# Performance work log

Measured on AMD Instinct MI355X. Metric: run time of the kernel, lower is better.

## Reference

```python
import jax, jax.numpy as jnp
import numpy as np

N_NODES = 100000
N_EDGES = 3200000
D_IN = 128
D_H0 = 64
D_H1 = 32
N_GRAPHS = 1024
N_CLASSES = 16


def setup_inputs() -> dict:
    key = jax.random.key(0)
    ks = jax.random.split(key, 9)
    x = jax.random.normal(ks[0], (N_NODES, D_IN), dtype=jnp.float32)
    edge_index = jax.random.randint(ks[1], (2, N_EDGES), 0, N_NODES, dtype=jnp.int64)
    node_graph_index = jnp.sort(
        jax.random.randint(ks[2], (N_NODES,), 0, N_GRAPHS, dtype=jnp.int64))

    def glorot(k, shape):
        lim = np.sqrt(6.0 / (shape[0] + shape[1]))
        return jax.random.uniform(k, shape, jnp.float32, -lim, lim)

    W0 = glorot(ks[3], (D_IN, D_H0))
    b0 = jnp.zeros((D_H0,), jnp.float32)
    W1 = glorot(ks[4], (D_H0, D_H1))
    b1 = jnp.zeros((D_H1,), jnp.float32)
    Wd = glorot(ks[5], (D_H1, N_CLASSES))
    bd = jnp.zeros((N_CLASSES,), jnp.float32)
    return {"x": x, "edge_index": edge_index, "node_graph_index": node_graph_index,
            "W0": W0, "b0": b0, "W1": W1, "b1": b1, "Wd": Wd, "bd": bd}


def reference(x, edge_index, node_graph_index, W0, b0, W1, b1, Wd, bd):
    N = x.shape[0]
    # GCN renormalization: add self-loops, symmetric D^-1/2 (A+I) D^-1/2
    loops = jnp.arange(N, dtype=edge_index.dtype)
    row = jnp.concatenate([edge_index[0], loops])  # target nodes
    col = jnp.concatenate([edge_index[1], loops])  # source nodes
    deg = jax.ops.segment_sum(jnp.ones_like(row, dtype=x.dtype), row, num_segments=N)
    inv_sqrt = jax.lax.rsqrt(deg)  # deg >= 1 thanks to self-loops
    norm = inv_sqrt[row] * inv_sqrt[col]  # [E+N]

    def gcn(h, W, b):
        hW = h @ W                                   # [N, d_out]
        msg = hW[col] * norm[:, None]                # [E+N, d_out]
        agg = jax.ops.segment_sum(msg, row, num_segments=N)
        return jax.nn.relu(agg + b)

    h = gcn(x, W0, b0)          # [N, 64]  (dropout is identity at inference)
    h = gcn(h, W1, b1)          # [N, 32]

    # mean pool over graphs
    sums = jax.ops.segment_sum(h, node_graph_index, num_segments=N_GRAPHS)
    cnt = jax.ops.segment_sum(jnp.ones((N,), x.dtype), node_graph_index,
                              num_segments=N_GRAPHS)
    pooled = sums / jnp.maximum(cnt, 1.0)[:, None]   # [G, 32]
    return pooled @ Wd + bd                          # [G, n_classes]
```

## Files before the change

### kernel.cpp

```cpp
#include <hip/hip_runtime.h>

#define GSHIFT 9
#define GSIZE 512
#define MAXG 256
#define GCAP 17664
#define CHUNKA 4096

typedef unsigned short bfraw;

__device__ __forceinline__ bfraw f2bf(float f) {
    unsigned u = __float_as_uint(f);
    unsigned r = u + 0x7FFFu + ((u >> 16) & 1u);
    return (bfraw)(r >> 16);
}
__device__ __forceinline__ float bflo(unsigned u) { return __uint_as_float(u << 16); }
__device__ __forceinline__ float bfhi(unsigned u) { return __uint_as_float(u & 0xFFFF0000u); }


__global__ __launch_bounds__(256) void k_ginit(int* __restrict__ gcur, int ngroups) {
    int g = threadIdx.x;
    if (g < ngroups) gcur[g] = g * GCAP;
}

__global__ __launch_bounds__(512) void k_partA(const int* __restrict__ row,
                                               const int* __restrict__ col,
                                               int* __restrict__ gcur,
                                               int* __restrict__ gbuf, int E) {
    __shared__ int h[MAXG];
    __shared__ int base[MAXG];
    int tid = threadIdx.x;
    if (tid < MAXG) h[tid] = 0;
    __syncthreads();
    int start = blockIdx.x * CHUNKA;
    int end = min(E, start + CHUNKA);
    for (int i = start + tid; i < end; i += 512)
        atomicAdd(&h[row[i] >> GSHIFT], 1);
    __syncthreads();
    if (tid < MAXG) {
        int c = h[tid];
        base[tid] = c ? atomicAdd(&gcur[tid], c) : 0;
        h[tid] = 0;
    }
    __syncthreads();
    for (int i = start + tid; i < end; i += 512) {
        int r = row[i], c = col[i];
        int g = r >> GSHIFT;
        int p = base[g] + atomicAdd(&h[g], 1);
        if (p < (g + 1) * GCAP)
            gbuf[p] = ((r & (GSIZE - 1)) << 17) | c;
    }
}

__global__ __launch_bounds__(512) void k_partB(const int* __restrict__ gbuf,
                                               const int* __restrict__ gcur,
                                               int* __restrict__ off,
                                               int* __restrict__ off2,
                                               int* __restrict__ scol,
                                               float* __restrict__ invs, int N) {
    __shared__ int hist[GSIZE];
    __shared__ int lex[GSIZE];
    int g = blockIdx.x, tid = threadIdx.x;
    int nstart = g << GSHIFT;
    int s = g * GCAP;
    int cnt = min(gcur[g] - s, GCAP);
    hist[tid] = 0;
    __syncthreads();
    for (int k = tid; k < cnt; k += 512)
        atomicAdd(&hist[gbuf[s + k] >> 17], 1);
    __syncthreads();
    int d0 = hist[tid];
    lex[tid] = d0;
    __syncthreads();
    for (int d = 1; d < GSIZE; d <<= 1) {
        int a = (tid >= d) ? lex[tid - d] : 0;
        __syncthreads();
        lex[tid] += a;
        __syncthreads();
    }
    int st = s + lex[tid] - d0;
    int node = nstart + tid;
    if (node < N) {
        off[node] = st;
        off2[node] = st + d0;
        invs[node] = rsqrtf((float)(d0 + 1));
    }
    hist[tid] = st;
    __syncthreads();
    for (int k = tid; k < cnt; k += 512) {
        int p = gbuf[s + k];
        int pos = atomicAdd(&hist[p >> 17], 1);
        scol[pos] = p & 0x1FFFF;
    }
}


__global__ __launch_bounds__(256) void k_gemm0(const float* __restrict__ x,
                                               const float* __restrict__ W,
                                               const float* __restrict__ invs,
                                               bfraw* __restrict__ out, int N) {
    __shared__ float sW[128 * 64];
    for (int i = threadIdx.x; i < 2048; i += 256)
        ((float4*)sW)[i] = ((const float4*)W)[i];
    __syncthreads();
    int t = threadIdx.x;
    int tc = t & 15, tr = t >> 4;
    int rbase = blockIdx.x * 64 + tr * 4;
    float acc[4][4] = {};
    int rr[4];
#pragma unroll
    for (int i = 0; i < 4; ++i) rr[i] = min(rbase + i, N - 1);
    for (int k = 0; k < 128; k += 4) {
        float4 wv0 = *(const float4*)&sW[(k + 0) * 64 + tc * 4];
        float4 wv1 = *(const float4*)&sW[(k + 1) * 64 + tc * 4];
        float4 wv2 = *(const float4*)&sW[(k + 2) * 64 + tc * 4];
        float4 wv3 = *(const float4*)&sW[(k + 3) * 64 + tc * 4];
#pragma unroll
        for (int i = 0; i < 4; ++i) {
            float4 xv = *(const float4*)(x + (size_t)rr[i] * 128 + k);
            acc[i][0] = fmaf(xv.x, wv0.x, acc[i][0]);
            acc[i][1] = fmaf(xv.x, wv0.y, acc[i][1]);
            acc[i][2] = fmaf(xv.x, wv0.z, acc[i][2]);
            acc[i][3] = fmaf(xv.x, wv0.w, acc[i][3]);
            acc[i][0] = fmaf(xv.y, wv1.x, acc[i][0]);
            acc[i][1] = fmaf(xv.y, wv1.y, acc[i][1]);
            acc[i][2] = fmaf(xv.y, wv1.z, acc[i][2]);
            acc[i][3] = fmaf(xv.y, wv1.w, acc[i][3]);
            acc[i][0] = fmaf(xv.z, wv2.x, acc[i][0]);
            acc[i][1] = fmaf(xv.z, wv2.y, acc[i][1]);
            acc[i][2] = fmaf(xv.z, wv2.z, acc[i][2]);
            acc[i][3] = fmaf(xv.z, wv2.w, acc[i][3]);
            acc[i][0] = fmaf(xv.w, wv3.x, acc[i][0]);
            acc[i][1] = fmaf(xv.w, wv3.y, acc[i][1]);
            acc[i][2] = fmaf(xv.w, wv3.z, acc[i][2]);
            acc[i][3] = fmaf(xv.w, wv3.w, acc[i][3]);
        }
    }
#pragma unroll
    for (int i = 0; i < 4; ++i) {
        int row = rbase + i;
        if (row < N) {
            float iv = invs[row];
            ushort4 o;
            o.x = f2bf(iv * acc[i][0]);
            o.y = f2bf(iv * acc[i][1]);
            o.z = f2bf(iv * acc[i][2]);
            o.w = f2bf(iv * acc[i][3]);
            *(ushort4*)(out + (size_t)row * 64 + tc * 4) = o;
        }
    }
}

__global__ __launch_bounds__(256) void k_gemm1(const float* __restrict__ h,
                                               const float* __restrict__ W,
                                               const float* __restrict__ invs,
                                               bfraw* __restrict__ out, int N) {
    __shared__ float sW[64 * 32];
    for (int i = threadIdx.x; i < 512; i += 256)
        ((float4*)sW)[i] = ((const float4*)W)[i];
    __syncthreads();
    int t = threadIdx.x;
    int tc = t & 7, tr = t >> 3;
    int rbase = blockIdx.x * 128 + tr * 4;
    float acc[4][4] = {};
    int rr[4];
#pragma unroll
    for (int i = 0; i < 4; ++i) rr[i] = min(rbase + i, N - 1);
    for (int k = 0; k < 64; k += 4) {
        float4 wv0 = *(const float4*)&sW[(k + 0) * 32 + tc * 4];
        float4 wv1 = *(const float4*)&sW[(k + 1) * 32 + tc * 4];
        float4 wv2 = *(const float4*)&sW[(k + 2) * 32 + tc * 4];
        float4 wv3 = *(const float4*)&sW[(k + 3) * 32 + tc * 4];
#pragma unroll
        for (int i = 0; i < 4; ++i) {
            float4 xv = *(const float4*)(h + (size_t)rr[i] * 64 + k);
            acc[i][0] = fmaf(xv.x, wv0.x, acc[i][0]);
            acc[i][1] = fmaf(xv.x, wv0.y, acc[i][1]);
            acc[i][2] = fmaf(xv.x, wv0.z, acc[i][2]);
            acc[i][3] = fmaf(xv.x, wv0.w, acc[i][3]);
            acc[i][0] = fmaf(xv.y, wv1.x, acc[i][0]);
            acc[i][1] = fmaf(xv.y, wv1.y, acc[i][1]);
            acc[i][2] = fmaf(xv.y, wv1.z, acc[i][2]);
            acc[i][3] = fmaf(xv.y, wv1.w, acc[i][3]);
            acc[i][0] = fmaf(xv.z, wv2.x, acc[i][0]);
            acc[i][1] = fmaf(xv.z, wv2.y, acc[i][1]);
            acc[i][2] = fmaf(xv.z, wv2.z, acc[i][2]);
            acc[i][3] = fmaf(xv.z, wv2.w, acc[i][3]);
            acc[i][0] = fmaf(xv.w, wv3.x, acc[i][0]);
            acc[i][1] = fmaf(xv.w, wv3.y, acc[i][1]);
            acc[i][2] = fmaf(xv.w, wv3.z, acc[i][2]);
            acc[i][3] = fmaf(xv.w, wv3.w, acc[i][3]);
        }
    }
#pragma unroll
    for (int i = 0; i < 4; ++i) {
        int row = rbase + i;
        if (row < N) {
            float iv = invs[row];
            ushort4 o;
            o.x = f2bf(iv * acc[i][0]);
            o.y = f2bf(iv * acc[i][1]);
            o.z = f2bf(iv * acc[i][2]);
            o.w = f2bf(iv * acc[i][3]);
            *(ushort4*)(out + (size_t)row * 32 + tc * 4) = o;
        }
    }
}


__global__ __launch_bounds__(256) void k_agg64_w(const int* __restrict__ scol,
                                                 const int* __restrict__ off,
                                                 const int* __restrict__ off2,
                                                 const float* __restrict__ invs,
                                                 const bfraw* __restrict__ hWb,
                                                 const float* __restrict__ bias,
                                                 float* __restrict__ h0, int N) {
    int node = blockIdx.x * 4 + (threadIdx.x >> 6);
    if (node >= N) return;
    int lane = threadIdx.x & 63;
    int fl = lane & 7, sg = lane >> 3;
    int s = off[node], e = off2[node];
    float a[8] = {}, c[8] = {};
    int k = s + sg;
    for (; k + 24 < e; k += 32) {
        int n0 = scol[k], n1 = scol[k + 8], n2 = scol[k + 16], n3 = scol[k + 24];
        uint4 u0 = *(const uint4*)(hWb + (size_t)n0 * 64 + fl * 8);
        uint4 u1 = *(const uint4*)(hWb + (size_t)n1 * 64 + fl * 8);
        uint4 u2 = *(const uint4*)(hWb + (size_t)n2 * 64 + fl * 8);
        uint4 u3 = *(const uint4*)(hWb + (size_t)n3 * 64 + fl * 8);
        a[0] += bflo(u0.x); a[1] += bfhi(u0.x); a[2] += bflo(u0.y); a[3] += bfhi(u0.y);
        a[4] += bflo(u0.z); a[5] += bfhi(u0.z); a[6] += bflo(u0.w); a[7] += bfhi(u0.w);
        c[0] += bflo(u1.x); c[1] += bfhi(u1.x); c[2] += bflo(u1.y); c[3] += bfhi(u1.y);
        c[4] += bflo(u1.z); c[5] += bfhi(u1.z); c[6] += bflo(u1.w); c[7] += bfhi(u1.w);
        a[0] += bflo(u2.x); a[1] += bfhi(u2.x); a[2] += bflo(u2.y); a[3] += bfhi(u2.y);
        a[4] += bflo(u2.z); a[5] += bfhi(u2.z); a[6] += bflo(u2.w); a[7] += bfhi(u2.w);
        c[0] += bflo(u3.x); c[1] += bfhi(u3.x); c[2] += bflo(u3.y); c[3] += bfhi(u3.y);
        c[4] += bflo(u3.z); c[5] += bfhi(u3.z); c[6] += bflo(u3.w); c[7] += bfhi(u3.w);
    }
    for (; k < e; k += 8) {
        uint4 u = *(const uint4*)(hWb + (size_t)scol[k] * 64 + fl * 8);
        a[0] += bflo(u.x); a[1] += bfhi(u.x); a[2] += bflo(u.y); a[3] += bfhi(u.y);
        a[4] += bflo(u.z); a[5] += bfhi(u.z); a[6] += bflo(u.w); a[7] += bfhi(u.w);
    }
#pragma unroll
    for (int j = 0; j < 8; ++j) a[j] += c[j];
#pragma unroll
    for (int m = 8; m < 64; m <<= 1) {
#pragma unroll
        for (int j = 0; j < 8; ++j) a[j] += __shfl_xor(a[j], m, 64);
    }
    if (sg == 0) {
        uint4 u = *(const uint4*)(hWb + (size_t)node * 64 + fl * 8);
        float iv = invs[node];
        int fb = fl * 8;
        float4 o1, o2;
        o1.x = fmaxf(iv * (a[0] + bflo(u.x)) + bias[fb + 0], 0.f);
        o1.y = fmaxf(iv * (a[1] + bfhi(u.x)) + bias[fb + 1], 0.f);
        o1.z = fmaxf(iv * (a[2] + bflo(u.y)) + bias[fb + 2], 0.f);
        o1.w = fmaxf(iv * (a[3] + bfhi(u.y)) + bias[fb + 3], 0.f);
        o2.x = fmaxf(iv * (a[4] + bflo(u.z)) + bias[fb + 4], 0.f);
        o2.y = fmaxf(iv * (a[5] + bfhi(u.z)) + bias[fb + 5], 0.f);
        o2.z = fmaxf(iv * (a[6] + bflo(u.w)) + bias[fb + 6], 0.f);
        o2.w = fmaxf(iv * (a[7] + bfhi(u.w)) + bias[fb + 7], 0.f);
        *(float4*)(h0 + (size_t)node * 64 + fb) = o1;
        *(float4*)(h0 + (size_t)node * 64 + fb + 4) = o2;
    }
}

__global__ __launch_bounds__(256) void k_agg32_w(const int* __restrict__ scol,
                                                 const int* __restrict__ off,
                                                 const int* __restrict__ off2,
                                                 const float* __restrict__ invs,
                                                 const bfraw* __restrict__ hWb,
                                                 const float* __restrict__ bias,
                                                 float* __restrict__ h1, int N) {
    int node = blockIdx.x * 4 + (threadIdx.x >> 6);
    if (node >= N) return;
    int lane = threadIdx.x & 63;
    int fl = lane & 3, sg = lane >> 2;
    int s = off[node], e = off2[node];
    float a[8] = {}, c[8] = {};
    int k = s + sg;
    for (; k + 16 < e; k += 32) {
        int n0 = scol[k], n1 = scol[k + 16];
        uint4 u0 = *(const uint4*)(hWb + (size_t)n0 * 32 + fl * 8);
        uint4 u1 = *(const uint4*)(hWb + (size_t)n1 * 32 + fl * 8);
        a[0] += bflo(u0.x); a[1] += bfhi(u0.x); a[2] += bflo(u0.y); a[3] += bfhi(u0.y);
        a[4] += bflo(u0.z); a[5] += bfhi(u0.z); a[6] += bflo(u0.w); a[7] += bfhi(u0.w);
        c[0] += bflo(u1.x); c[1] += bfhi(u1.x); c[2] += bflo(u1.y); c[3] += bfhi(u1.y);
        c[4] += bflo(u1.z); c[5] += bfhi(u1.z); c[6] += bflo(u1.w); c[7] += bfhi(u1.w);
    }
    for (; k < e; k += 16) {
        uint4 u = *(const uint4*)(hWb + (size_t)scol[k] * 32 + fl * 8);
        a[0] += bflo(u.x); a[1] += bfhi(u.x); a[2] += bflo(u.y); a[3] += bfhi(u.y);
        a[4] += bflo(u.z); a[5] += bfhi(u.z); a[6] += bflo(u.w); a[7] += bfhi(u.w);
    }
#pragma unroll
    for (int j = 0; j < 8; ++j) a[j] += c[j];
#pragma unroll
    for (int m = 4; m < 64; m <<= 1) {
#pragma unroll
        for (int j = 0; j < 8; ++j) a[j] += __shfl_xor(a[j], m, 64);
    }
    if (sg == 0) {
        uint4 u = *(const uint4*)(hWb + (size_t)node * 32 + fl * 8);
        float iv = invs[node];
        int fb = fl * 8;
        float4 o1, o2;
        o1.x = fmaxf(iv * (a[0] + bflo(u.x)) + bias[fb + 0], 0.f);
        o1.y = fmaxf(iv * (a[1] + bfhi(u.x)) + bias[fb + 1], 0.f);
        o1.z = fmaxf(iv * (a[2] + bflo(u.y)) + bias[fb + 2], 0.f);
        o1.w = fmaxf(iv * (a[3] + bfhi(u.y)) + bias[fb + 3], 0.f);
        o2.x = fmaxf(iv * (a[4] + bflo(u.z)) + bias[fb + 4], 0.f);
        o2.y = fmaxf(iv * (a[5] + bfhi(u.z)) + bias[fb + 5], 0.f);
        o2.z = fmaxf(iv * (a[6] + bflo(u.w)) + bias[fb + 6], 0.f);
        o2.w = fmaxf(iv * (a[7] + bfhi(u.w)) + bias[fb + 7], 0.f);
        *(float4*)(h1 + (size_t)node * 32 + fb) = o1;
        *(float4*)(h1 + (size_t)node * 32 + fb + 4) = o2;
    }
}


__global__ __launch_bounds__(256) void k_gbound(const int* __restrict__ gidx,
                                                int* __restrict__ gstart,
                                                int N, int G) {
    int i = blockIdx.x * 256 + threadIdx.x;
    if (i > N) return;
    if (i == 0) {
        int g0 = gidx[0];
        for (int g = 0; g <= g0; ++g) gstart[g] = 0;
    } else if (i == N) {
        int gl = gidx[N - 1];
        for (int g = gl + 1; g <= G; ++g) gstart[g] = N;
    } else {
        int a = gidx[i - 1], b = gidx[i];
        for (int g = a + 1; g <= b; ++g) gstart[g] = i;
    }
}

__global__ __launch_bounds__(256) void k_pool_head(const float* __restrict__ h1,
                                                   const int* __restrict__ gstart,
                                                   const float* __restrict__ Wd,
                                                   const float* __restrict__ bd,
                                                   float* __restrict__ out) {
    int g = blockIdx.x;
    int s = gstart[g], e = gstart[g + 1];
    int tid = threadIdx.x;
    int lane = tid & 63, w = tid >> 6;
    int f = lane & 31, half = lane >> 5;
    float acc = 0.f;
    for (int n = s + w * 2 + half; n < e; n += 8)
        acc += h1[(size_t)n * 32 + f];
    acc += __shfl_xor(acc, 32, 64);
    __shared__ float red[4][32];
    if (half == 0) red[w][f] = acc;
    __syncthreads();
    if (tid < 32) {
        float v = red[0][tid] + red[1][tid] + red[2][tid] + red[3][tid];
        red[0][tid] = v / fmaxf((float)(e - s), 1.0f);
    }
    __syncthreads();
    if (tid < 16) {
        float acc2 = bd[tid];
#pragma unroll
        for (int j = 0; j < 32; ++j)
            acc2 = fmaf(red[0][j], Wd[j * 16 + tid], acc2);
        out[g * 16 + tid] = acc2;
    }
}


static inline size_t align256(size_t v) { return (v + 255) & ~(size_t)255; }

extern "C" void kernel_launch(void* const* d_in, const int* in_sizes, int n_in,
                              void* d_out, int out_size, void* d_ws, size_t ws_size,
                              hipStream_t stream) {
    const float* x   = (const float*)d_in[0];
    const int*  erow = (const int*)d_in[1];
    const int*  gidx = (const int*)d_in[2];
    const float* W0  = (const float*)d_in[3];
    const float* b0  = (const float*)d_in[4];
    const float* W1  = (const float*)d_in[5];
    const float* b1  = (const float*)d_in[6];
    const float* Wd  = (const float*)d_in[7];
    const float* bd  = (const float*)d_in[8];
    float* out = (float*)d_out;

    const int E = in_sizes[1] / 2;
    const int* ecol = erow + E;
    const int N = in_sizes[2];
    const int G = out_size / 16;
    const int ngroups = (N + GSIZE - 1) / GSIZE;
    const int nchunks = (E + CHUNKA - 1) / CHUNKA;
    const size_t SLOTS = (size_t)ngroups * GCAP;

    char* ws = (char*)d_ws;
    size_t oInvs = 0;
    size_t oOff  = align256(oInvs + (size_t)N * 4);
    size_t oOff2 = align256(oOff + (size_t)N * 4);
    size_t oGc   = align256(oOff2 + (size_t)N * 4);
    size_t oScol = align256(oGc + (size_t)MAXG * 4);
    size_t oA    = align256(oScol + SLOTS * 4);
    size_t oB    = align256(oA + (size_t)N * 128);
    size_t oGs   = align256(oB + (size_t)N * 256);

    float* invs   = (float*)(ws + oInvs);
    int*   off    = (int*)(ws + oOff);
    int*   off2   = (int*)(ws + oOff2);
    int*   gcur   = (int*)(ws + oGc);
    int*   scol   = (int*)(ws + oScol);
    bfraw* tabA   = (bfraw*)(ws + oA);
    float* bufB   = (float*)(ws + oB);
    int*   gstart = (int*)(ws + oGs);
    int*   gbuf   = (int*)bufB;
    float* h1     = bufB;

    k_ginit<<<1, 256, 0, stream>>>(gcur, ngroups);
    k_partA<<<nchunks, 512, 0, stream>>>(erow, ecol, gcur, gbuf, E);
    k_partB<<<ngroups, 512, 0, stream>>>(gbuf, gcur, off, off2, scol, invs, N);

    k_gbound<<<(N + 256) / 256, 256, 0, stream>>>(gidx, gstart, N, G);

    k_gemm0<<<(N + 63) / 64, 256, 0, stream>>>(x, W0, invs, tabA, N);
    k_agg64_w<<<(N + 3) / 4, 256, 0, stream>>>(scol, off, off2, invs, tabA, b0, bufB, N);

    k_gemm1<<<(N + 127) / 128, 256, 0, stream>>>(bufB, W1, invs, tabA, N);
    k_agg32_w<<<(N + 3) / 4, 256, 0, stream>>>(scol, off, off2, invs, tabA, b1, h1, N);

    k_pool_head<<<G, 256, 0, stream>>>(h1, gstart, Wd, bd, out);
}
```

Measured before the change: 349.4 us.

## Stage edge partitioning in LDS for coalesced scatter, halve group size

The edge bucketing pass now counting-sorts each chunk in shared memory, using a block-wide scan over group counts, and then writes the sorted entries to the global group buffers. Runs of consecutive edges therefore go to the same group instead of scattering individually. The per-group CSR build also stages its sorted columns in shared memory before a coalesced copy out. Groups shrink to 256 nodes (512 groups) so each group's staging buffer fits in LDS. In exchange the kernels use more shared memory and extra barriers and scans, and row/col are read with int4 loads.

```diff
diff --git a/kernel.cpp b/kernel.cpp
--- a/kernel.cpp
+++ b/kernel.cpp
@@ -1,9 +1,9 @@
 #include <hip/hip_runtime.h>
 
-#define GSHIFT 9
-#define GSIZE 512
-#define MAXG 256
-#define GCAP 17664
+#define GSHIFT 8
+#define GSIZE 256
+#define MAXG 512
+#define GCAP 8960
 #define CHUNKA 4096
 
 typedef unsigned short bfraw;
@@ -17,7 +17,7 @@
 __device__ __forceinline__ float bfhi(unsigned u) { return __uint_as_float(u & 0xFFFF0000u); }
 
 
-__global__ __launch_bounds__(256) void k_ginit(int* __restrict__ gcur, int ngroups) {
+__global__ __launch_bounds__(512) void k_ginit(int* __restrict__ gcur, int ngroups) {
     int g = threadIdx.x;
     if (g < ngroups) gcur[g] = g * GCAP;
 }
@@ -25,29 +25,73 @@
 __global__ __launch_bounds__(512) void k_partA(const int* __restrict__ row,
                                                const int* __restrict__ col,
                                                int* __restrict__ gcur,
-                                               int* __restrict__ gbuf, int E) {
+                                               int* __restrict__ gbuf,
+                                               int E, int ngroups) {
     __shared__ int h[MAXG];
+    __shared__ int lst[MAXG];
     __shared__ int base[MAXG];
+    __shared__ int sorted[CHUNKA];
+    __shared__ int dstIdx[CHUNKA];
     int tid = threadIdx.x;
-    if (tid < MAXG) h[tid] = 0;
+    h[tid] = 0;
     __syncthreads();
     int start = blockIdx.x * CHUNKA;
     int end = min(E, start + CHUNKA);
-    for (int i = start + tid; i < end; i += 512)
-        atomicAdd(&h[row[i] >> GSHIFT], 1);
-    __syncthreads();
-    if (tid < MAXG) {
-        int c = h[tid];
-        base[tid] = c ? atomicAdd(&gcur[tid], c) : 0;
-        h[tid] = 0;
-    }
-    __syncthreads();
-    for (int i = start + tid; i < end; i += 512) {
-        int r = row[i], c = col[i];
-        int g = r >> GSHIFT;
-        int p = base[g] + atomicAdd(&h[g], 1);
-        if (p < (g + 1) * GCAP)
-            gbuf[p] = ((r & (GSIZE - 1)) << 17) | c;
+    for (int i = start + tid * 4; i < end; i += 2048) {
+        if (i + 3 < end) {
+            int4 r = *(const int4*)(row + i);
+            atomicAdd(&h[r.x >> GSHIFT], 1);
+            atomicAdd(&h[r.y >> GSHIFT], 1);
+            atomicAdd(&h[r.z >> GSHIFT], 1);
+            atomicAdd(&h[r.w >> GSHIFT], 1);
+        } else {
+            for (int j = i; j < end; ++j) atomicAdd(&h[row[j] >> GSHIFT], 1);
+        }
+    }
+    __syncthreads();
+    int v = h[tid];
+    lst[tid] = v;
+    __syncthreads();
+    for (int d = 1; d < MAXG; d <<= 1) {
+        int a = (tid >= d) ? lst[tid - d] : 0;
+        __syncthreads();
+        lst[tid] += a;
+        __syncthreads();
+    }
+    int excl = lst[tid] - v;
+    base[tid] = (v > 0 && tid < ngroups) ? atomicAdd(&gcur[tid], v) : 0;
+    lst[tid] = excl;
+    h[tid] = excl;
+    __syncthreads();
+    for (int i = start + tid * 4; i < end; i += 2048) {
+        if (i + 3 < end) {
+            int4 r = *(const int4*)(row + i);
+            int4 c = *(const int4*)(col + i);
+#pragma unroll
+            for (int j = 0; j < 4; ++j) {
+                int rr = (&r.x)[j], cc = (&c.x)[j];
+                int g = rr >> GSHIFT;
+                int p = atomicAdd(&h[g], 1);
+                sorted[p] = ((rr & (GSIZE - 1)) << 17) | cc;
+                int dst = base[g] + (p - lst[g]);
+                dstIdx[p] = (dst < (g + 1) * GCAP) ? dst : -1;
+            }
+        } else {
+            for (int j = i; j < end; ++j) {
+                int rr = row[j], cc = col[j];
+                int g = rr >> GSHIFT;
+                int p = atomicAdd(&h[g], 1);
+                sorted[p] = ((rr & (GSIZE - 1)) << 17) | cc;
+                int dst = base[g] + (p - lst[g]);
+                dstIdx[p] = (dst < (g + 1) * GCAP) ? dst : -1;
+            }
+        }
+    }
+    __syncthreads();
+    int cnt = end - start;
+    for (int i = tid; i < cnt; i += 512) {
+        int d = dstIdx[i];
+        if (d >= 0) gbuf[d] = sorted[i];
     }
 }
 
@@ -59,38 +103,43 @@
                                                float* __restrict__ invs, int N) {
     __shared__ int hist[GSIZE];
     __shared__ int lex[GSIZE];
+    __shared__ int sorted[GCAP];
     int g = blockIdx.x, tid = threadIdx.x;
-    int nstart = g << GSHIFT;
     int s = g * GCAP;
     int cnt = min(gcur[g] - s, GCAP);
-    hist[tid] = 0;
+    if (tid < GSIZE) hist[tid] = 0;
     __syncthreads();
     for (int k = tid; k < cnt; k += 512)
         atomicAdd(&hist[gbuf[s + k] >> 17], 1);
     __syncthreads();
-    int d0 = hist[tid];
-    lex[tid] = d0;
+    int d0 = (tid < GSIZE) ? hist[tid] : 0;
+    if (tid < GSIZE) lex[tid] = d0;
     __syncthreads();
     for (int d = 1; d < GSIZE; d <<= 1) {
-        int a = (tid >= d) ? lex[tid - d] : 0;
+        int a = 0;
+        if (tid < GSIZE && tid >= d) a = lex[tid - d];
         __syncthreads();
-        lex[tid] += a;
+        if (tid < GSIZE) lex[tid] += a;
         __syncthreads();
     }
-    int st = s + lex[tid] - d0;
-    int node = nstart + tid;
-    if (node < N) {
-        off[node] = st;
-        off2[node] = st + d0;
-        invs[node] = rsqrtf((float)(d0 + 1));
-    }
-    hist[tid] = st;
+    if (tid < GSIZE) {
+        int excl = lex[tid] - d0;
+        int node = (g << GSHIFT) + tid;
+        if (node < N) {
+            off[node] = s + excl;
+            off2[node] = s + excl + d0;
+            invs[node] = rsqrtf((float)(d0 + 1));
+        }
+        hist[tid] = excl;
+    }
     __syncthreads();
     for (int k = tid; k < cnt; k += 512) {
         int p = gbuf[s + k];
         int pos = atomicAdd(&hist[p >> 17], 1);
-        scol[pos] = p & 0x1FFFF;
-    }
+        sorted[pos] = p & 0x1FFFF;
+    }
+    __syncthreads();
+    for (int k = tid; k < cnt; k += 512) scol[s + k] = sorted[k];
 }
 
 
@@ -414,8 +463,8 @@
     int*   gbuf   = (int*)bufB;
     float* h1     = bufB;
 
-    k_ginit<<<1, 256, 0, stream>>>(gcur, ngroups);
-    k_partA<<<nchunks, 512, 0, stream>>>(erow, ecol, gcur, gbuf, E);
+    k_ginit<<<1, 512, 0, stream>>>(gcur, ngroups);
+    k_partA<<<nchunks, 512, 0, stream>>>(erow, ecol, gcur, gbuf, E, ngroups);
     k_partB<<<ngroups, 512, 0, stream>>>(gbuf, gcur, off, off2, scol, invs, N);
 
     k_gbound<<<(N + 256) / 256, 256, 0, stream>>>(gidx, gstart, N, G);
```

Result: faster. 324.4 us (-7.2%).
